# Performance work log

Measured on AMD Instinct MI355X. Metric: run time of the kernel, lower is better.

Reference implementation:

```python
import jax, jax.numpy as jnp
import numpy as np

N_NODES = 100000


def cheb_conv(x, src, dst, norm, W, b):
    # x: [N, F_in]; W: [K, F_in, F_out]; norm: [E]
    def prop(h):  # h -> L_hat @ h via edge scatter
        return jax.ops.segment_sum(norm[:, None] * h[src], dst, num_segments=N_NODES)

    K = W.shape[0]
    Tx0 = x
    out = Tx0 @ W[0]
    Tx1 = prop(x)
    out = out + Tx1 @ W[1]
    for k in range(2, K):
        Tx2 = 2.0 * prop(Tx1) - Tx0
        out = out + Tx2 @ W[k]
        Tx0, Tx1 = Tx1, Tx2
    return out + b


def setup_inputs() -> dict:
    key = jax.random.key(0)
    k1, k2, k3, k4 = jax.random.split(key, 4)
    F_in, H, C, K = 128, 64, 40, 3
    x = jax.random.normal(k1, (N_NODES, F_in), dtype=jnp.float32)
    edge_index = jax.random.randint(k2, (2, 1600000), 0, N_NODES, dtype=jnp.int64)
    W1 = jax.random.normal(k3, (K, F_in, H), dtype=jnp.float32) * 0.05
    b1 = jnp.zeros((H,), dtype=jnp.float32)
    W2 = jax.random.normal(k4, (K, H, C), dtype=jnp.float32) * 0.05
    b2 = jnp.zeros((C,), dtype=jnp.float32)
    return {"x": x, "edge_index": edge_index, "W1": W1, "b1": b1, "W2": W2, "b2": b2}


def reference(x, edge_index, W1, b1, W2, b2):
    src, dst = edge_index[0], edge_index[1]
    # sym-normalized scaled Laplacian L_hat = L - I = -D^{-1/2} A D^{-1/2} (lambda_max=2)
    deg = jax.ops.segment_sum(jnp.ones(src.shape[0], dtype=x.dtype), dst, num_segments=N_NODES)
    dis = jnp.where(deg > 0, jax.lax.rsqrt(jnp.where(deg > 0, deg, 1.0)), 0.0)
    norm = -dis[src] * dis[dst]

    h = cheb_conv(x, src, dst, norm, W1, b1)
    h = jax.nn.relu(h)
    # dropout is identity in eval mode
    h = cheb_conv(h, src, dst, norm, W2, b2)
    return jax.nn.log_softmax(h, axis=1)
```

## Files before the change

kernel.cpp:

```cpp
#include <hip/hip_runtime.h>
#include <hip/hip_bf16.h>
#include <math.h>


#define FIN1 128
#define HID 64
#define NCLS 40
#define CAP 48
#define NBUCK 512
#define NPB 196
#define BCAP 4096
#define EPB_A 8192

typedef __attribute__((ext_vector_type(8))) short sx8;
typedef __attribute__((ext_vector_type(4))) float fx4;

__device__ inline unsigned short f2bf(float f) {
    unsigned u = __float_as_uint(f);
    unsigned r = (u + 0x7FFF + ((u >> 16) & 1)) >> 16;
    return (unsigned short)r;
}
__device__ inline float bf2f(unsigned short h) {
    return __uint_as_float((unsigned)h << 16);
}
__device__ inline unsigned pack2bf(float a, float b) {
    return (unsigned)f2bf(a) | ((unsigned)f2bf(b) << 16);
}
__device__ inline float lo2f(unsigned v) { return __uint_as_float(v << 16); }
__device__ inline float hi2f(unsigned v) { return __uint_as_float(v & 0xffff0000u); }
__device__ inline float deg2dis(int dg) {
    return (dg > 0) ? rsqrtf((float)dg) : 0.0f;
}

__global__ __launch_bounds__(256) void k_passA(const int* __restrict__ src,
                                               const int* __restrict__ dst, int E,
                                               int* __restrict__ bcursor,
                                               unsigned* __restrict__ bbuf) {
    __shared__ int hist[NBUCK];
    __shared__ int gbase[NBUCK];
    __shared__ int cnt2[NBUCK];
    int t = threadIdx.x;
    for (int i = t; i < NBUCK; i += 256) {
        hist[i] = 0;
        cnt2[i] = 0;
    }
    __syncthreads();
    int e0 = blockIdx.x * EPB_A;
    int e1 = min(e0 + EPB_A, E);
    for (int e = e0 + t; e < e1; e += 256) {
        int bin = (unsigned)dst[e] / NPB;
        atomicAdd(&hist[bin], 1);
    }
    __syncthreads();
    for (int i = t; i < NBUCK; i += 256)
        gbase[i] = (hist[i] > 0) ? atomicAdd(&bcursor[i], hist[i]) : 0;
    __syncthreads();
    for (int e = e0 + t; e < e1; e += 256) {
        int d = dst[e];
        int bin = (unsigned)d / NPB;
        int rank = atomicAdd(&cnt2[bin], 1);
        int pos = gbase[bin] + rank;
        if (pos < BCAP)
            bbuf[(size_t)bin * BCAP + pos] =
                ((unsigned)(d - bin * NPB) << 17) | (unsigned)src[e];
    }
}

__global__ __launch_bounds__(256) void k_passB(const int* __restrict__ bcursor,
                                               const unsigned* __restrict__ bbuf,
                                               unsigned* __restrict__ csr,
                                               int* __restrict__ count, int N) {
    __shared__ int cnt[NPB];
    __shared__ unsigned loc[NPB * CAP];
    int b = blockIdx.x;
    int t = threadIdx.x;
    for (int i = t; i < NPB; i += 256) cnt[i] = 0;
    __syncthreads();
    int ne = min(bcursor[b], BCAP);
    for (int i = t; i < ne; i += 256) {
        unsigned v = bbuf[(size_t)b * BCAP + i];
        int d = v >> 17;
        int rank = atomicAdd(&cnt[d], 1);
        if (rank < CAP) loc[d * CAP + rank] = v & 0x1FFFFu;
    }
    __syncthreads();
    int node0 = b * NPB;
    for (int i = t; i < NPB; i += 256) {
        int node = node0 + i;
        if (node < N) count[node] = min(cnt[i], CAP);
    }
    for (int i = t; i < NPB * CAP; i += 256) {
        int node = node0 + i / CAP;
        if (node < N) csr[(size_t)node0 * CAP + i] = loc[i];
    }
}

template <int NS, int T, int FIN, int FOE>
__global__ void k_wprep(const float* __restrict__ W, unsigned short* __restrict__ hi,
                        unsigned short* __restrict__ lo) {
    int idx = blockIdx.x * 256 + threadIdx.x;
    constexpr int total = NS * T * 64 * 8;
    if (idx >= total) return;
    int i = idx & 7;
    int l = (idx >> 3) & 63;
    int t = (idx >> 9) % T;
    int s = idx / (512 * T);
    int k = s * 32 + (l >> 4) * 8 + i;
    int col = t * 16 + (l & 15);
    float w = 0.0f;
    if (col < 3 * FOE) {
        int m = col / FOE;
        int c = col - m * FOE;
        if (m == 0)
            w = W[((size_t)0 * FIN + k) * FOE + c] - W[((size_t)2 * FIN + k) * FOE + c];
        else
            w = W[((size_t)m * FIN + k) * FOE + c];
    }
    unsigned short h = f2bf(w);
    hi[idx] = h;
    lo[idx] = f2bf(w - bf2f(h));
}

template <int FIN, int T, int NS, int FOE>
__global__ __launch_bounds__(256, 6) void k_gemm_mfma(
    const float* __restrict__ A, const unsigned short* __restrict__ Whi,
    const unsigned short* __restrict__ Wlo, const int* __restrict__ count,
    unsigned short* __restrict__ OHd, unsigned short* __restrict__ OHa,
    unsigned short* __restrict__ Th, int N) {
    int tid = threadIdx.x;
    int w = tid >> 6, l = tid & 63;
    int row0 = blockIdx.x * 64 + w * 16;
    int rl = l & 15, kg = l >> 4;

    fx4 acc[T];
#pragma unroll
    for (int t = 0; t < T; ++t) acc[t] = (fx4)0.0f;

    for (int s = 0; s < NS; ++s) {
        int k0 = s * 32 + kg * 8;
        int r = min(row0 + rl, N - 1);
        const fx4* ap = (const fx4*)(A + (size_t)r * FIN + k0);
        fx4 a0 = ap[0];
        fx4 a1 = ap[1];
        sx8 ahi, alo;
#pragma unroll
        for (int j = 0; j < 4; ++j) {
            unsigned short h0 = f2bf(a0[j]);
            unsigned short h1 = f2bf(a1[j]);
            ahi[j] = (short)h0;
            ahi[j + 4] = (short)h1;
            alo[j] = (short)f2bf(a0[j] - bf2f(h0));
            alo[j + 4] = (short)f2bf(a1[j] - bf2f(h1));
        }
        const sx8* wh = (const sx8*)(Whi + ((size_t)(s * T) * 64 + l) * 8);
        const sx8* wl = (const sx8*)(Wlo + ((size_t)(s * T) * 64 + l) * 8);
#pragma unroll
        for (int t = 0; t < T; ++t) {
            sx8 bh = wh[t * 64];
            sx8 bl = wl[t * 64];
            acc[t] = __builtin_amdgcn_mfma_f32_16x16x32_bf16(ahi, bh, acc[t], 0, 0, 0);
            acc[t] = __builtin_amdgcn_mfma_f32_16x16x32_bf16(ahi, bl, acc[t], 0, 0, 0);
            acc[t] = __builtin_amdgcn_mfma_f32_16x16x32_bf16(alo, bh, acc[t], 0, 0, 0);
        }
    }

    float ds_[4];
#pragma unroll
    for (int j = 0; j < 4; ++j)
        ds_[j] = deg2dis(count[min(row0 + kg * 4 + j, N - 1)]);

#pragma unroll
    for (int t = 0; t < T; ++t) {
        int col = t * 16 + rl;
        int m = col / FOE;
        int cc = col - m * FOE;
        if (m < 3) {
#pragma unroll
            for (int j = 0; j < 4; ++j) {
                int r = row0 + kg * 4 + j;
                if (r < N) {
                    if (m == 0) OHd[(size_t)r * 64 + cc] = f2bf(acc[t][j]);
                    else if (m == 1) OHa[(size_t)r * 64 + cc] = f2bf(acc[t][j]);
                    else Th[(size_t)r * 64 + cc] = f2bf(ds_[j] * acc[t][j]);
                }
            }
        }
    }
}

template <int FIN, int T, int NS, int FOE>
__global__ __launch_bounds__(256, 6) void k_gemm_mfma_bf(
    const unsigned short* __restrict__ A, const unsigned short* __restrict__ Whi,
    const unsigned short* __restrict__ Wlo, const int* __restrict__ count,
    float* __restrict__ C0, unsigned short* __restrict__ OHa,
    unsigned short* __restrict__ Th, int N) {
    int tid = threadIdx.x;
    int w = tid >> 6, l = tid & 63;
    int row0 = blockIdx.x * 64 + w * 16;
    int rl = l & 15, kg = l >> 4;

    fx4 acc[T];
#pragma unroll
    for (int t = 0; t < T; ++t) acc[t] = (fx4)0.0f;

    for (int s = 0; s < NS; ++s) {
        int k0 = s * 32 + kg * 8;
        int r = min(row0 + rl, N - 1);
        sx8 a = *(const sx8*)(A + (size_t)r * FIN + k0);
        const sx8* wh = (const sx8*)(Whi + ((size_t)(s * T) * 64 + l) * 8);
        const sx8* wl = (const sx8*)(Wlo + ((size_t)(s * T) * 64 + l) * 8);
#pragma unroll
        for (int t = 0; t < T; ++t) {
            sx8 bh = wh[t * 64];
            sx8 bl = wl[t * 64];
            acc[t] = __builtin_amdgcn_mfma_f32_16x16x32_bf16(a, bh, acc[t], 0, 0, 0);
            acc[t] = __builtin_amdgcn_mfma_f32_16x16x32_bf16(a, bl, acc[t], 0, 0, 0);
        }
    }

    float ds_[4];
#pragma unroll
    for (int j = 0; j < 4; ++j)
        ds_[j] = deg2dis(count[min(row0 + kg * 4 + j, N - 1)]);

#pragma unroll
    for (int t = 0; t < T; ++t) {
        int col = t * 16 + rl;
        int m = col / FOE;
        int cc = col - m * FOE;
        if (m < 3) {
#pragma unroll
            for (int j = 0; j < 4; ++j) {
                int r = row0 + kg * 4 + j;
                if (r < N) {
                    if (m == 0) C0[(size_t)r * FOE + cc] = acc[t][j];
                    else if (m == 1) OHa[(size_t)r * 64 + cc] = f2bf(acc[t][j]);
                    else Th[(size_t)r * 64 + cc] = f2bf(ds_[j] * acc[t][j]);
                }
            }
        }
    }
}

template <int F, int MODE>
__global__ void k_prop(const int* __restrict__ count,
                       const unsigned* __restrict__ csr,
                       const unsigned* __restrict__ tab,
                       const unsigned* __restrict__ oh,
                       const float* __restrict__ o0f,
                       const float* __restrict__ bias,
                       unsigned* __restrict__ outh, float* __restrict__ outf, int N) {
    constexpr int FH = F / 2;
    int wid = (blockIdx.x * blockDim.x + threadIdx.x) >> 6;
    int lane = threadIdx.x & 63;
    if (wid >= N) return;
    int g = lane >> 5;
    int c = lane & 31;
    int cnt = count[wid];
    float wd = deg2dis(cnt);
    int md = (int)csr[(size_t)wid * CAP + min(lane, CAP - 1)];
    md = (lane < cnt) ? md : N;
    int g4 = g << 2;
    float ax = 0.0f, ay = 0.0f;

#define PSTEP(T_)                                                          \
    {                                                                      \
        int s_ = __builtin_amdgcn_ds_bpermute(((T_) * 2) * 4 + g4, md);    \
        unsigned off_ = (unsigned)s_ * 32u + (unsigned)c;                  \
        unsigned v_ = (c < FH) ? tab[off_] : 0u;                           \
        ax += lo2f(v_);                                                    \
        ay += hi2f(v_);                                                    \
    }

#pragma unroll
    for (int t = 0; t < 8; ++t) PSTEP(t);
    if (cnt > 16) {
#pragma unroll
        for (int t = 8; t < 16; ++t) PSTEP(t);
        if (cnt > 32) {
#pragma unroll
            for (int t = 16; t < 24; ++t) PSTEP(t);
        }
    }
#undef PSTEP

    ax += __shfl_xor(ax, 32);
    ay += __shfl_xor(ay, 32);

    if (MODE == 0) {
        if (g == 0 && c < FH) {
            unsigned ov = oh[(size_t)wid * 32 + c];
            float s0 = lo2f(ov) - 2.0f * wd * ax;
            float s1 = hi2f(ov) - 2.0f * wd * ay;
            outh[(size_t)wid * 32 + c] = pack2bf(wd * s0, wd * s1);
        }
    } else if (MODE == 1) {
        if (g == 0 && c < FH) {
            unsigned ov = oh[(size_t)wid * 32 + c];
            float2 b = ((const float2*)bias)[c];
            float z0 = fmaxf(lo2f(ov) - wd * ax + b.x, 0.0f);
            float z1 = fmaxf(hi2f(ov) - wd * ay + b.y, 0.0f);
            outh[(size_t)wid * 32 + c] = pack2bf(z0, z1);
        }
    } else {
        float z0 = -INFINITY, z1 = -INFINITY;
        if (g == 0 && c < FH) {
            float2 o = ((const float2*)o0f)[(size_t)wid * FH + c];
            float2 b = ((const float2*)bias)[c];
            z0 = o.x - wd * ax + b.x;
            z1 = o.y - wd * ay + b.y;
        }
        float m = fmaxf(z0, z1);
#pragma unroll
        for (int d = 32; d; d >>= 1) m = fmaxf(m, __shfl_xor(m, d));
        float e0 = (g == 0 && c < FH) ? expf(z0 - m) : 0.0f;
        float e1 = (g == 0 && c < FH) ? expf(z1 - m) : 0.0f;
        float l = e0 + e1;
#pragma unroll
        for (int d = 32; d; d >>= 1) l += __shfl_xor(l, d);
        if (g == 0 && c < FH) {
            float lg = m + logf(l);
            ((float2*)outf)[(size_t)wid * FH + c] = make_float2(z0 - lg, z1 - lg);
        }
    }
}

extern "C" void kernel_launch(void* const* d_in, const int* in_sizes, int n_in,
                              void* d_out, int out_size, void* d_ws, size_t ws_size,
                              hipStream_t stream) {
    const float* x = (const float*)d_in[0];
    const int* ei = (const int*)d_in[1];
    const float* W1 = (const float*)d_in[2];
    const float* b1 = (const float*)d_in[3];
    const float* W2 = (const float*)d_in[4];
    const float* b2 = (const float*)d_in[5];
    float* out = (float*)d_out;

    const int N = in_sizes[0] / FIN1;
    const int E = in_sizes[1] / 2;
    const int* src = ei;
    const int* dst = ei + E;

    char* p = (char*)d_ws;
    auto alloc = [&](size_t bytes) -> void* {
        void* r = (void*)p;
        p += (bytes + 255) & ~(size_t)255;
        return r;
    };
    int* count = (int*)alloc((size_t)N * 4);
    int* bcursor = (int*)alloc((size_t)NBUCK * 4);
    unsigned* bbuf = (unsigned*)alloc((size_t)NBUCK * BCAP * 4);
    unsigned* csr = (unsigned*)alloc((size_t)N * CAP * 4);
    float* buf0 = (float*)alloc((size_t)N * NCLS * 4);
    unsigned* blkA = (unsigned*)alloc((size_t)(N + 1) * 32 * 4);
    unsigned* blkB = (unsigned*)alloc((size_t)(N + 1) * 32 * 4);
    unsigned* bufDD = (unsigned*)alloc((size_t)N * 32 * 4);
    unsigned* bufCA = (unsigned*)alloc((size_t)N * 32 * 4);
    unsigned* buf4h = (unsigned*)alloc((size_t)N * 32 * 4);
    constexpr int W1FRAG = 4 * 12 * 64 * 8;
    constexpr int W2FRAG = 2 * 8 * 64 * 8;
    unsigned short* wf1h = (unsigned short*)alloc((size_t)W1FRAG * 2);
    unsigned short* wf1l = (unsigned short*)alloc((size_t)W1FRAG * 2);
    unsigned short* wf2h = (unsigned short*)alloc((size_t)W2FRAG * 2);
    unsigned short* wf2l = (unsigned short*)alloc((size_t)W2FRAG * 2);

    const int bg = (N + 63) / 64;
    const int bp = (N * 64 + 255) / 256;
    const int ba = (E + EPB_A - 1) / EPB_A;
    const int bb = (N + NPB - 1) / NPB;

    k_wprep<4, 12, FIN1, HID><<<(W1FRAG + 255) / 256, 256, 0, stream>>>(W1, wf1h, wf1l);
    k_wprep<2, 8, HID, NCLS><<<(W2FRAG + 255) / 256, 256, 0, stream>>>(W2, wf2h, wf2l);

    hipMemsetAsync(blkA + (size_t)N * 32, 0, 128, stream);
    hipMemsetAsync(blkB + (size_t)N * 32, 0, 128, stream);

    hipMemsetAsync(bcursor, 0, (size_t)NBUCK * 4, stream);
    k_passA<<<ba, 256, 0, stream>>>(src, dst, E, bcursor, bbuf);
    k_passB<<<bb, 256, 0, stream>>>(bcursor, bbuf, csr, count, N);

    k_gemm_mfma<FIN1, 12, 4, HID><<<bg, 256, 0, stream>>>(
        x, wf1h, wf1l, count, (unsigned short*)bufDD, (unsigned short*)bufCA,
        (unsigned short*)blkA, N);
    k_prop<HID, 0><<<bp, 256, 0, stream>>>(count, csr, blkA, bufCA, nullptr,
                                           nullptr, blkB, nullptr, N);
    k_prop<HID, 1><<<bp, 256, 0, stream>>>(count, csr, blkB, bufDD, nullptr,
                                           b1, buf4h, nullptr, N);

    k_gemm_mfma_bf<HID, 8, 2, NCLS><<<bg, 256, 0, stream>>>(
        (const unsigned short*)buf4h, wf2h, wf2l, count, buf0,
        (unsigned short*)bufDD, (unsigned short*)blkA, N);
    k_prop<NCLS, 0><<<bp, 256, 0, stream>>>(count, csr, blkA, bufDD, nullptr,
                                            nullptr, blkB, nullptr, N);
    k_prop<NCLS, 2><<<bp, 256, 0, stream>>>(count, csr, blkB, nullptr,
                                            buf0, b2, nullptr, out, N);
}
```

Before: 267.4 us.

## Drop A low-part split in first GEMM, preload A rows, relax launch bounds

The fp32-input GEMM no longer splits activations into bf16 hi/lo halves. It converts them once with the hardware packed bf16 convert and issues two MFMAs per tile instead of three. Both GEMM kernels now load all K-slices of their A row up front into registers, and the occupancy hint drops from 6 to 4 waves so the extra registers fit. This cuts conversion ALU work and one MFMA per tile and hides load latency, but lowers the precision of the first layer's product and may reduce occupancy.

```diff
diff --git a/kernel.cpp b/kernel.cpp
--- a/kernel.cpp
+++ b/kernel.cpp
@@ -14,6 +14,7 @@
 
 typedef __attribute__((ext_vector_type(8))) short sx8;
 typedef __attribute__((ext_vector_type(4))) float fx4;
+typedef __attribute__((ext_vector_type(4))) unsigned ux4;
 
 __device__ inline unsigned short f2bf(float f) {
     unsigned u = __float_as_uint(f);
@@ -30,6 +31,11 @@
 __device__ inline float hi2f(unsigned v) { return __uint_as_float(v & 0xffff0000u); }
 __device__ inline float deg2dis(int dg) {
     return (dg > 0) ? rsqrtf((float)dg) : 0.0f;
+}
+__device__ inline unsigned cvtpk(float a, float b) {
+    unsigned r;
+    asm("v_cvt_pk_bf16_f32 %0, %1, %2" : "=v"(r) : "v"(a), "v"(b));
+    return r;
 }
 
 __global__ __launch_bounds__(256) void k_passA(const int* __restrict__ src,
@@ -122,7 +128,7 @@
 }
 
 template <int FIN, int T, int NS, int FOE>
-__global__ __launch_bounds__(256, 6) void k_gemm_mfma(
+__global__ __launch_bounds__(256, 4) void k_gemm_mfma(
     const float* __restrict__ A, const unsigned short* __restrict__ Whi,
     const unsigned short* __restrict__ Wlo, const int* __restrict__ count,
     unsigned short* __restrict__ OHd, unsigned short* __restrict__ OHa,
@@ -132,35 +138,36 @@
     int row0 = blockIdx.x * 64 + w * 16;
     int rl = l & 15, kg = l >> 4;
 
+    int r = min(row0 + rl, N - 1);
+    const float* arow = A + (size_t)r * FIN + kg * 8;
+    fx4 a0s[NS], a1s[NS];
+#pragma unroll
+    for (int s = 0; s < NS; ++s) {
+        const fx4* ap = (const fx4*)(arow + s * 32);
+        a0s[s] = ap[0];
+        a1s[s] = ap[1];
+    }
+
     fx4 acc[T];
 #pragma unroll
     for (int t = 0; t < T; ++t) acc[t] = (fx4)0.0f;
 
+#pragma unroll
     for (int s = 0; s < NS; ++s) {
-        int k0 = s * 32 + kg * 8;
-        int r = min(row0 + rl, N - 1);
-        const fx4* ap = (const fx4*)(A + (size_t)r * FIN + k0);
-        fx4 a0 = ap[0];
-        fx4 a1 = ap[1];
-        sx8 ahi, alo;
-#pragma unroll
-        for (int j = 0; j < 4; ++j) {
-            unsigned short h0 = f2bf(a0[j]);
-            unsigned short h1 = f2bf(a1[j]);
-            ahi[j] = (short)h0;
-            ahi[j + 4] = (short)h1;
-            alo[j] = (short)f2bf(a0[j] - bf2f(h0));
-            alo[j + 4] = (short)f2bf(a1[j] - bf2f(h1));
-        }
+        ux4 uu;
+        uu.x = cvtpk(a0s[s][0], a0s[s][1]);
+        uu.y = cvtpk(a0s[s][2], a0s[s][3]);
+        uu.z = cvtpk(a1s[s][0], a1s[s][1]);
+        uu.w = cvtpk(a1s[s][2], a1s[s][3]);
+        sx8 ah = __builtin_bit_cast(sx8, uu);
         const sx8* wh = (const sx8*)(Whi + ((size_t)(s * T) * 64 + l) * 8);
         const sx8* wl = (const sx8*)(Wlo + ((size_t)(s * T) * 64 + l) * 8);
 #pragma unroll
         for (int t = 0; t < T; ++t) {
             sx8 bh = wh[t * 64];
             sx8 bl = wl[t * 64];
-            acc[t] = __builtin_amdgcn_mfma_f32_16x16x32_bf16(ahi, bh, acc[t], 0, 0, 0);
-            acc[t] = __builtin_amdgcn_mfma_f32_16x16x32_bf16(ahi, bl, acc[t], 0, 0, 0);
-            acc[t] = __builtin_amdgcn_mfma_f32_16x16x32_bf16(alo, bh, acc[t], 0, 0, 0);
+            acc[t] = __builtin_amdgcn_mfma_f32_16x16x32_bf16(ah, bh, acc[t], 0, 0, 0);
+            acc[t] = __builtin_amdgcn_mfma_f32_16x16x32_bf16(ah, bl, acc[t], 0, 0, 0);
         }
     }
 
@@ -177,11 +184,11 @@
         if (m < 3) {
 #pragma unroll
             for (int j = 0; j < 4; ++j) {
-                int r = row0 + kg * 4 + j;
-                if (r < N) {
-                    if (m == 0) OHd[(size_t)r * 64 + cc] = f2bf(acc[t][j]);
-                    else if (m == 1) OHa[(size_t)r * 64 + cc] = f2bf(acc[t][j]);
-                    else Th[(size_t)r * 64 + cc] = f2bf(ds_[j] * acc[t][j]);
+                int r2 = row0 + kg * 4 + j;
+                if (r2 < N) {
+                    if (m == 0) OHd[(size_t)r2 * 64 + cc] = f2bf(acc[t][j]);
+                    else if (m == 1) OHa[(size_t)r2 * 64 + cc] = f2bf(acc[t][j]);
+                    else Th[(size_t)r2 * 64 + cc] = f2bf(ds_[j] * acc[t][j]);
                 }
             }
         }
@@ -189,7 +196,7 @@
 }
 
 template <int FIN, int T, int NS, int FOE>
-__global__ __launch_bounds__(256, 6) void k_gemm_mfma_bf(
+__global__ __launch_bounds__(256, 4) void k_gemm_mfma_bf(
     const unsigned short* __restrict__ A, const unsigned short* __restrict__ Whi,
     const unsigned short* __restrict__ Wlo, const int* __restrict__ count,
     float* __restrict__ C0, unsigned short* __restrict__ OHa,
@@ -199,22 +206,26 @@
     int row0 = blockIdx.x * 64 + w * 16;
     int rl = l & 15, kg = l >> 4;
 
+    int r = min(row0 + rl, N - 1);
+    sx8 a_s[NS];
+#pragma unroll
+    for (int s = 0; s < NS; ++s)
+        a_s[s] = *(const sx8*)(A + (size_t)r * FIN + s * 32 + kg * 8);
+
     fx4 acc[T];
 #pragma unroll
     for (int t = 0; t < T; ++t) acc[t] = (fx4)0.0f;
 
+#pragma unroll
     for (int s = 0; s < NS; ++s) {
-        int k0 = s * 32 + kg * 8;
-        int r = min(row0 + rl, N - 1);
-        sx8 a = *(const sx8*)(A + (size_t)r * FIN + k0);
         const sx8* wh = (const sx8*)(Whi + ((size_t)(s * T) * 64 + l) * 8);
         const sx8* wl = (const sx8*)(Wlo + ((size_t)(s * T) * 64 + l) * 8);
 #pragma unroll
         for (int t = 0; t < T; ++t) {
             sx8 bh = wh[t * 64];
             sx8 bl = wl[t * 64];
-            acc[t] = __builtin_amdgcn_mfma_f32_16x16x32_bf16(a, bh, acc[t], 0, 0, 0);
-            acc[t] = __builtin_amdgcn_mfma_f32_16x16x32_bf16(a, bl, acc[t], 0, 0, 0);
+            acc[t] = __builtin_amdgcn_mfma_f32_16x16x32_bf16(a_s[s], bh, acc[t], 0, 0, 0);
+            acc[t] = __builtin_amdgcn_mfma_f32_16x16x32_bf16(a_s[s], bl, acc[t], 0, 0, 0);
         }
     }
 
@@ -231,11 +242,11 @@
         if (m < 3) {
 #pragma unroll
             for (int j = 0; j < 4; ++j) {
-                int r = row0 + kg * 4 + j;
-                if (r < N) {
-                    if (m == 0) C0[(size_t)r * FOE + cc] = acc[t][j];
-                    else if (m == 1) OHa[(size_t)r * 64 + cc] = f2bf(acc[t][j]);
-                    else Th[(size_t)r * 64 + cc] = f2bf(ds_[j] * acc[t][j]);
+                int r2 = row0 + kg * 4 + j;
+                if (r2 < N) {
+                    if (m == 0) C0[(size_t)r2 * FOE + cc] = acc[t][j];
+                    else if (m == 1) OHa[(size_t)r2 * 64 + cc] = f2bf(acc[t][j]);
+                    else Th[(size_t)r2 * 64 + cc] = f2bf(ds_[j] * acc[t][j]);
                 }
             }
         }
```

Result: faster. 258.5 us (-3.3%).
